# Kernel optimization log

Measured on AMD Instinct MI355X. Metric: run time of the kernel, lower is better.

Reference implementation:

```python
import jax, jax.numpy as jnp
import numpy as np

EPS = 1e-12  # matches torch F.normalize eps


def setup_inputs() -> dict:
    key = jax.random.key(0)
    k_x, k_w, k_b, k_c, k_f = jax.random.split(key, 5)
    N, C, H, W = 32, 128, 64, 64
    K = 64
    x = jax.random.normal(k_x, (N, C, H, W), dtype=jnp.float32)
    conv_w = jax.random.normal(k_w, (K, C), dtype=jnp.float32) * 0.05  # 1x1 conv weight [K,C,1,1] squeezed
    conv_b = jax.random.normal(k_b, (K,), dtype=jnp.float32) * 0.05
    centroids = jax.random.uniform(k_c, (K, C), dtype=jnp.float32)
    fc_w = jax.random.normal(k_f, (1, K), dtype=jnp.float32) * 0.1  # nn.Linear(K,1,bias=False).weight
    return {"x": x, "conv_w": conv_w, "conv_b": conv_b, "centroids": centroids, "fc_w": fc_w}


def _l2norm(v, axis):
    return v / jnp.maximum(jnp.linalg.norm(v, axis=axis, keepdims=True), EPS)


def reference(x, conv_w, conv_b, centroids, fc_w):
    N, C, H, W = x.shape
    K = conv_w.shape[0]
    # descriptor-wise L2 normalize over channel dim
    x = _l2norm(x, axis=1)
    xf = x.reshape(N, C, H * W)                                   # [N,C,S]
    # 1x1 conv == per-pixel linear over channels
    logits = jnp.einsum('kc,ncs->nks', conv_w, xf) + conv_b[None, :, None]
    a = jax.nn.softmax(logits, axis=1)                            # [N,K,S] soft assignment
    # VLAD: sum_s a[n,k,s] * (x[n,:,s] - centroids[k,:]), loop-free
    vlad = jnp.einsum('nks,ncs->nkc', a, xf) \
           - a.sum(axis=-1)[..., None] * centroids[None, :, :]    # [N,K,C]
    # intra-normalization over descriptor dim
    vlad = _l2norm(vlad, axis=2)
    # lastfc: [N,C,K] @ [K] -> [N,C]
    out = jnp.einsum('nkc,k->nc', vlad, fc_w[0])
    return out
```

## Files before the change

kernel.cpp:

```cpp
#include <hip/hip_runtime.h>
#include <math.h>

#define Nn 32
#define Cc 128
#define Ss 4096
#define Kk 64
#define NCHUNK 16
#define SCHUNK (Ss / NCHUNK)
#define ST 64
#define NSUB (SCHUNK / ST)
#define BLK 256

#define XCS 72
#define XTS 136
#define LKS 68
#define AS  72
#define RS  17

typedef __attribute__((ext_vector_type(8))) short short8;
typedef __attribute__((ext_vector_type(4))) float float4v;

__device__ __forceinline__ unsigned f2bf(float f) {
    unsigned u = __builtin_bit_cast(unsigned, f);
    return (u + 0x7fffu + ((u >> 16) & 1u)) >> 16;
}
__device__ __forceinline__ unsigned pack2(float a, float b) {
    return f2bf(a) | (f2bf(b) << 16);
}

__global__ __launch_bounds__(BLK, 2) void netvlad_main(
    const float* __restrict__ x,
    const float* __restrict__ conv_w,
    const float* __restrict__ conv_b,
    float* __restrict__ vlad,
    float* __restrict__ asum)
{
    __shared__ __align__(16) unsigned short xC[Cc * XCS];
    __shared__ __align__(16) float Lbuf[ST * LKS];
    __shared__ __align__(16) unsigned short aB[Kk * AS];
    __shared__ float red[ST * RS];
    __shared__ float invn[ST];
    unsigned short* xT = (unsigned short*)Lbuf;

    const int t    = threadIdx.x;
    const int n    = blockIdx.y;
    const int w    = t >> 6;
    const int l    = t & 63;
    const int m    = l & 15;
    const int quad = l >> 4;
    const int p    = t >> 2;
    const int ii   = t & 3;

    short8 wfrag[4];
    {
        const float* wr_ = conv_w + (16 * w + m) * Cc;
#pragma unroll
        for (int ks = 0; ks < 4; ++ks) {
            float4 wa = *(const float4*)(wr_ + 32 * ks + 8 * quad);
            float4 wb = *(const float4*)(wr_ + 32 * ks + 8 * quad + 4);
            union { short8 s8; unsigned u[4]; } W_;
            W_.u[0] = pack2(wa.x, wa.y);
            W_.u[1] = pack2(wa.z, wa.w);
            W_.u[2] = pack2(wb.x, wb.y);
            W_.u[3] = pack2(wb.z, wb.w);
            wfrag[ks] = W_.s8;
        }
    }
    float bias_r[4];
#pragma unroll
    for (int r = 0; r < 4; ++r) bias_r[r] = conv_b[16 * w + 4 * quad + r];

    float4v acc[8];
#pragma unroll
    for (int nt = 0; nt < 8; ++nt) acc[nt] = (float4v){0.f, 0.f, 0.f, 0.f};
    float asum_part[16];
#pragma unroll
    for (int j = 0; j < 16; ++j) asum_part[j] = 0.f;

    const float* xn = x + (size_t)n * Cc * Ss;

    for (int sub = 0; sub < NSUB; ++sub) {
        const int s0 = blockIdx.x * SCHUNK + sub * ST;
        __syncthreads();

        {
            float sp0 = 0.f, sp1 = 0.f, sp2 = 0.f, sp3 = 0.f;
            const int sq = (t & 15) << 2;
#pragma unroll
            for (int r = 0; r < 8; ++r) {
                int c = (t >> 4) + 16 * r;
                float4 v = *(const float4*)(xn + (size_t)c * Ss + s0 + sq);
                sp0 += v.x * v.x; sp1 += v.y * v.y;
                sp2 += v.z * v.z; sp3 += v.w * v.w;
                uint2 pk = make_uint2(pack2(v.x, v.y), pack2(v.z, v.w));
                *(uint2*)&xC[c * XCS + sq] = pk;
            }
            red[(sq + 0) * RS + (t >> 4)] = sp0;
            red[(sq + 1) * RS + (t >> 4)] = sp1;
            red[(sq + 2) * RS + (t >> 4)] = sp2;
            red[(sq + 3) * RS + (t >> 4)] = sp3;
        }
        __syncthreads();

        if (t < ST) {
            float tot = 0.f;
#pragma unroll
            for (int i = 0; i < 16; ++i) tot += red[t * RS + i];
            invn[t] = 1.0f / fmaxf(sqrtf(tot), 1e-12f);
        }
        {
            int s = t & 63, oct0 = t >> 6;
#pragma unroll
            for (int q = 0; q < 4; ++q) {
                int oct = oct0 + 4 * q;
                uint4 dd;
                dd.x = (unsigned)xC[(8 * oct + 0) * XCS + s] | ((unsigned)xC[(8 * oct + 1) * XCS + s] << 16);
                dd.y = (unsigned)xC[(8 * oct + 2) * XCS + s] | ((unsigned)xC[(8 * oct + 3) * XCS + s] << 16);
                dd.z = (unsigned)xC[(8 * oct + 4) * XCS + s] | ((unsigned)xC[(8 * oct + 5) * XCS + s] << 16);
                dd.w = (unsigned)xC[(8 * oct + 6) * XCS + s] | ((unsigned)xC[(8 * oct + 7) * XCS + s] << 16);
                *(uint4*)&xT[s * XTS + 8 * oct] = dd;
            }
        }
        __syncthreads();

        float4v Lr[4];
#pragma unroll
        for (int nt = 0; nt < 4; ++nt) Lr[nt] = (float4v){0.f, 0.f, 0.f, 0.f};
#pragma unroll
        for (int nt = 0; nt < 4; ++nt) {
#pragma unroll
            for (int ks = 0; ks < 4; ++ks) {
                short8 b = *(const short8*)&xT[(16 * nt + m) * XTS + 32 * ks + 8 * quad];
                Lr[nt] = __builtin_amdgcn_mfma_f32_16x16x32_bf16(wfrag[ks], b, Lr[nt], 0, 0, 0);
            }
        }
        __syncthreads();

#pragma unroll
        for (int nt = 0; nt < 4; ++nt) {
            float iv = invn[16 * nt + m];
            float4 o;
            o.x = Lr[nt].x * iv + bias_r[0];
            o.y = Lr[nt].y * iv + bias_r[1];
            o.z = Lr[nt].z * iv + bias_r[2];
            o.w = Lr[nt].w * iv + bias_r[3];
            *(float4*)&Lbuf[(16 * nt + m) * LKS + 16 * w + 4 * quad] = o;
        }
        __syncthreads();

        {
            float lv[16];
#pragma unroll
            for (int j = 0; j < 16; ++j) lv[j] = Lbuf[p * LKS + ii + 4 * j];
            float mx = lv[0];
#pragma unroll
            for (int j = 1; j < 16; ++j) mx = fmaxf(mx, lv[j]);
            mx = fmaxf(mx, __shfl_xor(mx, 1));
            mx = fmaxf(mx, __shfl_xor(mx, 2));
            float e[16];
            float lsum = 0.f;
#pragma unroll
            for (int j = 0; j < 16; ++j) { e[j] = __expf(lv[j] - mx); lsum += e[j]; }
            lsum += __shfl_xor(lsum, 1);
            lsum += __shfl_xor(lsum, 2);
            float itot = 1.0f / lsum;
            float sca  = itot * invn[p];
#pragma unroll
            for (int j = 0; j < 16; ++j) {
                float av = e[j] * itot;
                asum_part[j] += av;
                aB[(ii + 4 * j) * AS + p] = (unsigned short)f2bf(e[j] * sca);
            }
        }
        __syncthreads();

#pragma unroll
        for (int ks = 0; ks < 2; ++ks) {
            short8 af = *(const short8*)&aB[(16 * w + m) * AS + 32 * ks + 8 * quad];
#pragma unroll
            for (int nt = 0; nt < 8; ++nt) {
                short8 bf_ = *(const short8*)&xC[(16 * nt + m) * XCS + 32 * ks + 8 * quad];
                acc[nt] = __builtin_amdgcn_mfma_f32_16x16x32_bf16(af, bf_, acc[nt], 0, 0, 0);
            }
        }
    }

    float* vb = vlad + ((size_t)n * Kk + 16 * w + 4 * quad) * Cc + m;
#pragma unroll
    for (int nt = 0; nt < 8; ++nt) {
        atomicAdd(vb + 0 * Cc + 16 * nt, acc[nt].x);
        atomicAdd(vb + 1 * Cc + 16 * nt, acc[nt].y);
        atomicAdd(vb + 2 * Cc + 16 * nt, acc[nt].z);
        atomicAdd(vb + 3 * Cc + 16 * nt, acc[nt].w);
    }

    __syncthreads();
#pragma unroll
    for (int j = 0; j < 16; ++j) Lbuf[p * LKS + ii + 4 * j] = asum_part[j];
    __syncthreads();
    if (t < Kk) {
        float s_ = 0.f;
        for (int p2 = 0; p2 < ST; ++p2) s_ += Lbuf[p2 * LKS + t];
        atomicAdd(&asum[n * Kk + t], s_);
    }
}

__global__ __launch_bounds__(256) void netvlad_final(
    const float* __restrict__ vlad, const float* __restrict__ asum,
    const float* __restrict__ centroids, const float* __restrict__ fc_w,
    float* __restrict__ out)
{
    __shared__ float scale_s[Kk];
    __shared__ float asum_s[Kk];
    __shared__ float red2[Kk][4];

    const int n = blockIdx.x;
    const int t = threadIdx.x;
    const int k = t >> 2;
    const int q = t & 3;

    const float* vr = vlad + ((size_t)n * Kk + k) * Cc + q * 32;
    const float* cr = centroids + k * Cc + q * 32;
    const float  as = asum[n * Kk + k];

    float ssq = 0.f;
#pragma unroll
    for (int i = 0; i < 8; ++i) {
        float4 v4 = *(const float4*)(vr + 4 * i);
        float4 c4 = *(const float4*)(cr + 4 * i);
        float d0 = v4.x - as * c4.x;
        float d1 = v4.y - as * c4.y;
        float d2 = v4.z - as * c4.z;
        float d3 = v4.w - as * c4.w;
        ssq += d0 * d0 + d1 * d1 + d2 * d2 + d3 * d3;
    }
    red2[k][q] = ssq;
    __syncthreads();
    if (q == 0) {
        float tot = red2[k][0] + red2[k][1] + red2[k][2] + red2[k][3];
        scale_s[k] = fc_w[k] / fmaxf(sqrtf(tot), 1e-12f);
        asum_s[k]  = as;
    }
    __syncthreads();

    if (t < Cc) {
        const int c = t;
        const float* vbp = vlad + (size_t)n * Kk * Cc + c;
        float o = 0.f;
#pragma unroll 8
        for (int k2 = 0; k2 < Kk; ++k2)
            o += scale_s[k2] * (vbp[k2 * Cc] - asum_s[k2] * centroids[k2 * Cc + c]);
        out[n * Cc + c] = o;
    }
}

extern "C" void kernel_launch(void* const* d_in, const int* in_sizes, int n_in,
                              void* d_out, int out_size, void* d_ws, size_t ws_size,
                              hipStream_t stream) {
    (void)in_sizes; (void)n_in; (void)out_size; (void)ws_size;
    const float* x         = (const float*)d_in[0];
    const float* conv_w    = (const float*)d_in[1];
    const float* conv_b    = (const float*)d_in[2];
    const float* centroids = (const float*)d_in[3];
    const float* fc_w      = (const float*)d_in[4];
    float* out = (float*)d_out;

    float* vlad = (float*)d_ws;
    float* asum = vlad + (size_t)Nn * Kk * Cc;
    size_t zero_bytes = ((size_t)Nn * Kk * Cc + (size_t)Nn * Kk) * sizeof(float);
    hipMemsetAsync(d_ws, 0, zero_bytes, stream);

    dim3 grid(NCHUNK, Nn);
    netvlad_main<<<grid, BLK, 0, stream>>>(x, conv_w, conv_b, vlad, asum);
    netvlad_final<<<Nn, 256, 0, stream>>>(vlad, asum, centroids, fc_w, out);
}
```

Measured before the change: 120.4 us.

## Fuse main and final kernels via cooperative grid sync with per-chunk partials

Replaces the memset, the atomic-accumulating main kernel and the final kernel with one cooperative kernel. Each block writes its per-chunk VLAD and assignment-sum partials without atomics, then after a grid sync 256 blocks reduce the partials, normalize and atomically add into the output, which block 0 zeroes up front. A fallback two-kernel path is kept in case the cooperative launch fails. This removes launch and memset overhead and atomic contention, but relies on all 512 blocks being co-resident, adds a grid barrier, and writes a 16x larger partial buffer.

Measured after the change: 256.5 us. 113% more time.

```diff
diff --git a/kernel.cpp b/kernel.cpp
--- a/kernel.cpp
+++ b/kernel.cpp
@@ -1,5 +1,8 @@
 #include <hip/hip_runtime.h>
+#include <hip/hip_cooperative_groups.h>
 #include <math.h>
+
+namespace cg = cooperative_groups;
 
 #define Nn 32
 #define Cc 128
@@ -20,6 +23,14 @@
 typedef __attribute__((ext_vector_type(8))) short short8;
 typedef __attribute__((ext_vector_type(4))) float float4v;
 
+struct __align__(16) LdsA {
+    unsigned short xC[Cc * XCS];
+    float Lbuf[ST * LKS];
+    unsigned short aB[Kk * AS];
+    float red[ST * RS];
+    float invn[ST];
+};
+
 __device__ __forceinline__ unsigned f2bf(float f) {
     unsigned u = __builtin_bit_cast(unsigned, f);
     return (u + 0x7fffu + ((u >> 16) & 1u)) >> 16;
@@ -28,22 +39,18 @@
     return f2bf(a) | (f2bf(b) << 16);
 }
 
-__global__ __launch_bounds__(BLK, 2) void netvlad_main(
+__device__ __forceinline__ void run_phaseA(
+    LdsA& S,
     const float* __restrict__ x,
     const float* __restrict__ conv_w,
     const float* __restrict__ conv_b,
-    float* __restrict__ vlad,
-    float* __restrict__ asum)
-{
-    __shared__ __align__(16) unsigned short xC[Cc * XCS];
-    __shared__ __align__(16) float Lbuf[ST * LKS];
-    __shared__ __align__(16) unsigned short aB[Kk * AS];
-    __shared__ float red[ST * RS];
-    __shared__ float invn[ST];
-    unsigned short* xT = (unsigned short*)Lbuf;
+    float* __restrict__ vladp,
+    float* __restrict__ asump,
+    int chunk, int n)
+{
+    unsigned short* xT = (unsigned short*)S.Lbuf;
 
     const int t    = threadIdx.x;
-    const int n    = blockIdx.y;
     const int w    = t >> 6;
     const int l    = t & 63;
     const int m    = l & 15;
@@ -80,7 +87,7 @@
     const float* xn = x + (size_t)n * Cc * Ss;
 
     for (int sub = 0; sub < NSUB; ++sub) {
-        const int s0 = blockIdx.x * SCHUNK + sub * ST;
+        const int s0 = chunk * SCHUNK + sub * ST;
         __syncthreads();
 
         {
@@ -93,20 +100,20 @@
                 sp0 += v.x * v.x; sp1 += v.y * v.y;
                 sp2 += v.z * v.z; sp3 += v.w * v.w;
                 uint2 pk = make_uint2(pack2(v.x, v.y), pack2(v.z, v.w));
-                *(uint2*)&xC[c * XCS + sq] = pk;
-            }
-            red[(sq + 0) * RS + (t >> 4)] = sp0;
-            red[(sq + 1) * RS + (t >> 4)] = sp1;
-            red[(sq + 2) * RS + (t >> 4)] = sp2;
-            red[(sq + 3) * RS + (t >> 4)] = sp3;
+                *(uint2*)&S.xC[c * XCS + sq] = pk;
+            }
+            S.red[(sq + 0) * RS + (t >> 4)] = sp0;
+            S.red[(sq + 1) * RS + (t >> 4)] = sp1;
+            S.red[(sq + 2) * RS + (t >> 4)] = sp2;
+            S.red[(sq + 3) * RS + (t >> 4)] = sp3;
         }
         __syncthreads();
 
         if (t < ST) {
             float tot = 0.f;
 #pragma unroll
-            for (int i = 0; i < 16; ++i) tot += red[t * RS + i];
-            invn[t] = 1.0f / fmaxf(sqrtf(tot), 1e-12f);
+            for (int i = 0; i < 16; ++i) tot += S.red[t * RS + i];
+            S.invn[t] = 1.0f / fmaxf(sqrtf(tot), 1e-12f);
         }
         {
             int s = t & 63, oct0 = t >> 6;
@@ -114,10 +121,10 @@
             for (int q = 0; q < 4; ++q) {
                 int oct = oct0 + 4 * q;
                 uint4 dd;
-                dd.x = (unsigned)xC[(8 * oct + 0) * XCS + s] | ((unsigned)xC[(8 * oct + 1) * XCS + s] << 16);
-                dd.y = (unsigned)xC[(8 * oct + 2) * XCS + s] | ((unsigned)xC[(8 * oct + 3) * XCS + s] << 16);
-                dd.z = (unsigned)xC[(8 * oct + 4) * XCS + s] | ((unsigned)xC[(8 * oct + 5) * XCS + s] << 16);
-                dd.w = (unsigned)xC[(8 * oct + 6) * XCS + s] | ((unsigned)xC[(8 * oct + 7) * XCS + s] << 16);
+                dd.x = (unsigned)S.xC[(8 * oct + 0) * XCS + s] | ((unsigned)S.xC[(8 * oct + 1) * XCS + s] << 16);
+                dd.y = (unsigned)S.xC[(8 * oct + 2) * XCS + s] | ((unsigned)S.xC[(8 * oct + 3) * XCS + s] << 16);
+                dd.z = (unsigned)S.xC[(8 * oct + 4) * XCS + s] | ((unsigned)S.xC[(8 * oct + 5) * XCS + s] << 16);
+                dd.w = (unsigned)S.xC[(8 * oct + 6) * XCS + s] | ((unsigned)S.xC[(8 * oct + 7) * XCS + s] << 16);
                 *(uint4*)&xT[s * XTS + 8 * oct] = dd;
             }
         }
@@ -138,20 +145,20 @@
 
 #pragma unroll
         for (int nt = 0; nt < 4; ++nt) {
-            float iv = invn[16 * nt + m];
+            float iv = S.invn[16 * nt + m];
             float4 o;
             o.x = Lr[nt].x * iv + bias_r[0];
             o.y = Lr[nt].y * iv + bias_r[1];
             o.z = Lr[nt].z * iv + bias_r[2];
             o.w = Lr[nt].w * iv + bias_r[3];
-            *(float4*)&Lbuf[(16 * nt + m) * LKS + 16 * w + 4 * quad] = o;
+            *(float4*)&S.Lbuf[(16 * nt + m) * LKS + 16 * w + 4 * quad] = o;
         }
         __syncthreads();
 
         {
             float lv[16];
 #pragma unroll
-            for (int j = 0; j < 16; ++j) lv[j] = Lbuf[p * LKS + ii + 4 * j];
+            for (int j = 0; j < 16; ++j) lv[j] = S.Lbuf[p * LKS + ii + 4 * j];
             float mx = lv[0];
 #pragma unroll
             for (int j = 1; j < 16; ++j) mx = fmaxf(mx, lv[j]);
@@ -164,94 +171,169 @@
             lsum += __shfl_xor(lsum, 1);
             lsum += __shfl_xor(lsum, 2);
             float itot = 1.0f / lsum;
-            float sca  = itot * invn[p];
+            float sca  = itot * S.invn[p];
 #pragma unroll
             for (int j = 0; j < 16; ++j) {
                 float av = e[j] * itot;
                 asum_part[j] += av;
-                aB[(ii + 4 * j) * AS + p] = (unsigned short)f2bf(e[j] * sca);
+                S.aB[(ii + 4 * j) * AS + p] = (unsigned short)f2bf(e[j] * sca);
             }
         }
         __syncthreads();
 
 #pragma unroll
         for (int ks = 0; ks < 2; ++ks) {
-            short8 af = *(const short8*)&aB[(16 * w + m) * AS + 32 * ks + 8 * quad];
+            short8 af = *(const short8*)&S.aB[(16 * w + m) * AS + 32 * ks + 8 * quad];
 #pragma unroll
             for (int nt = 0; nt < 8; ++nt) {
-                short8 bf_ = *(const short8*)&xC[(16 * nt + m) * XCS + 32 * ks + 8 * quad];
+                short8 bf_ = *(const short8*)&S.xC[(16 * nt + m) * XCS + 32 * ks + 8 * quad];
                 acc[nt] = __builtin_amdgcn_mfma_f32_16x16x32_bf16(af, bf_, acc[nt], 0, 0, 0);
             }
         }
     }
 
-    float* vb = vlad + ((size_t)n * Kk + 16 * w + 4 * quad) * Cc + m;
-#pragma unroll
-    for (int nt = 0; nt < 8; ++nt) {
-        atomicAdd(vb + 0 * Cc + 16 * nt, acc[nt].x);
-        atomicAdd(vb + 1 * Cc + 16 * nt, acc[nt].y);
-        atomicAdd(vb + 2 * Cc + 16 * nt, acc[nt].z);
-        atomicAdd(vb + 3 * Cc + 16 * nt, acc[nt].w);
-    }
-
-    __syncthreads();
-#pragma unroll
-    for (int j = 0; j < 16; ++j) Lbuf[p * LKS + ii + 4 * j] = asum_part[j];
+    {
+        float* vb = vladp + ((((size_t)chunk * Nn + n) * Kk) + 16 * w + 4 * quad) * Cc + m;
+#pragma unroll
+        for (int nt = 0; nt < 8; ++nt) {
+            vb[0 * Cc + 16 * nt] = acc[nt].x;
+            vb[1 * Cc + 16 * nt] = acc[nt].y;
+            vb[2 * Cc + 16 * nt] = acc[nt].z;
+            vb[3 * Cc + 16 * nt] = acc[nt].w;
+        }
+    }
+
+    __syncthreads();
+#pragma unroll
+    for (int j = 0; j < 16; ++j) S.Lbuf[p * LKS + ii + 4 * j] = asum_part[j];
     __syncthreads();
     if (t < Kk) {
         float s_ = 0.f;
-        for (int p2 = 0; p2 < ST; ++p2) s_ += Lbuf[p2 * LKS + t];
-        atomicAdd(&asum[n * Kk + t], s_);
-    }
-}
-
-__global__ __launch_bounds__(256) void netvlad_final(
-    const float* __restrict__ vlad, const float* __restrict__ asum,
-    const float* __restrict__ centroids, const float* __restrict__ fc_w,
+        for (int p2 = 0; p2 < ST; ++p2) s_ += S.Lbuf[p2 * LKS + t];
+        asump[((size_t)chunk * Nn + n) * Kk + t] = s_;
+    }
+}
+
+__device__ __forceinline__ void run_phaseB(
+    LdsA& S,
+    const float* __restrict__ vladp,
+    const float* __restrict__ asump,
+    const float* __restrict__ centroids,
+    const float* __restrict__ fc_w,
+    float* __restrict__ out,
+    int bid)
+{
+    const int t  = threadIdx.x;
+    const int n2 = bid >> 3;
+    const int kg = bid & 7;
+    const int kl = t >> 5;
+    const int c4 = t & 31;
+    const int k2 = 8 * kg + kl;
+
+    float* asum_s  = (float*)S.aB;
+    float* scale_s = asum_s + 8;
+    float4* osum   = (float4*)S.xC;
+
+    float4 v = make_float4(0.f, 0.f, 0.f, 0.f);
+    const float* vp = vladp + ((size_t)n2 * Kk + k2) * Cc + 4 * c4;
+#pragma unroll
+    for (int ch = 0; ch < NCHUNK; ++ch) {
+        float4 u = *(const float4*)(vp + (size_t)ch * Nn * Kk * Cc);
+        v.x += u.x; v.y += u.y; v.z += u.z; v.w += u.w;
+    }
+    if (t < 8) {
+        float a = 0.f;
+#pragma unroll
+        for (int ch = 0; ch < NCHUNK; ++ch)
+            a += asump[((size_t)ch * Nn + n2) * Kk + 8 * kg + t];
+        asum_s[t] = a;
+    }
+    __syncthreads();
+
+    const float a2 = asum_s[kl];
+    float4 cv = *(const float4*)(centroids + (size_t)k2 * Cc + 4 * c4);
+    float dx = v.x - a2 * cv.x;
+    float dy = v.y - a2 * cv.y;
+    float dz = v.z - a2 * cv.z;
+    float dw = v.w - a2 * cv.w;
+
+    float ssq = dx * dx + dy * dy + dz * dz + dw * dw;
+    ssq += __shfl_xor(ssq, 1);
+    ssq += __shfl_xor(ssq, 2);
+    ssq += __shfl_xor(ssq, 4);
+    ssq += __shfl_xor(ssq, 8);
+    ssq += __shfl_xor(ssq, 16);
+    if ((t & 31) == 0)
+        scale_s[kl] = fc_w[k2] / fmaxf(sqrtf(ssq), 1e-12f);
+    __syncthreads();
+
+    const float sc = scale_s[kl];
+    osum[kl * 32 + c4] = make_float4(sc * dx, sc * dy, sc * dz, sc * dw);
+    __syncthreads();
+
+    if (t < 32) {
+        float4 tot = osum[t];
+#pragma unroll
+        for (int kl2 = 1; kl2 < 8; ++kl2) {
+            float4 o2 = osum[kl2 * 32 + t];
+            tot.x += o2.x; tot.y += o2.y; tot.z += o2.z; tot.w += o2.w;
+        }
+        atomicAdd(&out[n2 * Cc + 4 * t + 0], tot.x);
+        atomicAdd(&out[n2 * Cc + 4 * t + 1], tot.y);
+        atomicAdd(&out[n2 * Cc + 4 * t + 2], tot.z);
+        atomicAdd(&out[n2 * Cc + 4 * t + 3], tot.w);
+    }
+}
+
+__global__ __launch_bounds__(BLK, 3) void netvlad_fused(
+    const float* __restrict__ x,
+    const float* __restrict__ conv_w,
+    const float* __restrict__ conv_b,
+    const float* __restrict__ centroids,
+    const float* __restrict__ fc_w,
+    float* __restrict__ out,
+    float* __restrict__ vladp,
+    float* __restrict__ asump)
+{
+    __shared__ LdsA S;
+    const int bid = blockIdx.y * NCHUNK + blockIdx.x;
+
+    if (bid == 0) {
+        float4 z4 = make_float4(0.f, 0.f, 0.f, 0.f);
+#pragma unroll
+        for (int i = 0; i < 4; ++i)
+            ((float4*)out)[threadIdx.x + 256 * i] = z4;
+    }
+
+    run_phaseA(S, x, conv_w, conv_b, vladp, asump, blockIdx.x, blockIdx.y);
+
+    __threadfence();
+    cg::this_grid().sync();
+
+    if (bid < Nn * 8)
+        run_phaseB(S, vladp, asump, centroids, fc_w, out, bid);
+}
+
+__global__ __launch_bounds__(BLK, 3) void netvlad_pA(
+    const float* __restrict__ x,
+    const float* __restrict__ conv_w,
+    const float* __restrict__ conv_b,
+    float* __restrict__ vladp,
+    float* __restrict__ asump)
+{
+    __shared__ LdsA S;
+    run_phaseA(S, x, conv_w, conv_b, vladp, asump, blockIdx.x, blockIdx.y);
+}
+
+__global__ __launch_bounds__(BLK) void netvlad_pB(
+    const float* __restrict__ vladp,
+    const float* __restrict__ asump,
+    const float* __restrict__ centroids,
+    const float* __restrict__ fc_w,
     float* __restrict__ out)
 {
-    __shared__ float scale_s[Kk];
-    __shared__ float asum_s[Kk];
-    __shared__ float red2[Kk][4];
-
-    const int n = blockIdx.x;
-    const int t = threadIdx.x;
-    const int k = t >> 2;
-    const int q = t & 3;
-
-    const float* vr = vlad + ((size_t)n * Kk + k) * Cc + q * 32;
-    const float* cr = centroids + k * Cc + q * 32;
-    const float  as = asum[n * Kk + k];
-
-    float ssq = 0.f;
-#pragma unroll
-    for (int i = 0; i < 8; ++i) {
-        float4 v4 = *(const float4*)(vr + 4 * i);
-        float4 c4 = *(const float4*)(cr + 4 * i);
-        float d0 = v4.x - as * c4.x;
-        float d1 = v4.y - as * c4.y;
-        float d2 = v4.z - as * c4.z;
-        float d3 = v4.w - as * c4.w;
-        ssq += d0 * d0 + d1 * d1 + d2 * d2 + d3 * d3;
-    }
-    red2[k][q] = ssq;
-    __syncthreads();
-    if (q == 0) {
-        float tot = red2[k][0] + red2[k][1] + red2[k][2] + red2[k][3];
-        scale_s[k] = fc_w[k] / fmaxf(sqrtf(tot), 1e-12f);
-        asum_s[k]  = as;
-    }
-    __syncthreads();
-
-    if (t < Cc) {
-        const int c = t;
-        const float* vbp = vlad + (size_t)n * Kk * Cc + c;
-        float o = 0.f;
-#pragma unroll 8
-        for (int k2 = 0; k2 < Kk; ++k2)
-            o += scale_s[k2] * (vbp[k2 * Cc] - asum_s[k2] * centroids[k2 * Cc + c]);
-        out[n * Cc + c] = o;
-    }
+    __shared__ LdsA S;
+    run_phaseB(S, vladp, asump, centroids, fc_w, out, blockIdx.x);
 }
 
 extern "C" void kernel_launch(void* const* d_in, const int* in_sizes, int n_in,
@@ -265,12 +347,18 @@
     const float* fc_w      = (const float*)d_in[4];
     float* out = (float*)d_out;
 
-    float* vlad = (float*)d_ws;
-    float* asum = vlad + (size_t)Nn * Kk * Cc;
-    size_t zero_bytes = ((size_t)Nn * Kk * Cc + (size_t)Nn * Kk) * sizeof(float);
-    hipMemsetAsync(d_ws, 0, zero_bytes, stream);
+    float* vladp = (float*)d_ws;
+    float* asump = vladp + (size_t)NCHUNK * Nn * Kk * Cc;
 
     dim3 grid(NCHUNK, Nn);
-    netvlad_main<<<grid, BLK, 0, stream>>>(x, conv_w, conv_b, vlad, asum);
-    netvlad_final<<<Nn, 256, 0, stream>>>(vlad, asum, centroids, fc_w, out);
-}
+    dim3 block(BLK);
+    void* args[] = {(void*)&x, (void*)&conv_w, (void*)&conv_b, (void*)&centroids,
+                    (void*)&fc_w, (void*)&out, (void*)&vladp, (void*)&asump};
+    hipError_t rc = hipLaunchCooperativeKernel((void*)netvlad_fused, grid, block,
+                                               args, 0, stream);
+    if (rc != hipSuccess) {
+        hipMemsetAsync(out, 0, (size_t)Nn * Cc * sizeof(float), stream);
+        netvlad_pA<<<grid, block, 0, stream>>>(x, conv_w, conv_b, vladp, asump);
+        netvlad_pB<<<dim3(Nn * 8), block, 0, stream>>>(vladp, asump, centroids, fc_w, out);
+    }
+}
```
